# Optimization experiments

Hardware: AMD Instinct MI355X
Metric: run time of the kernel (lower is better)

## Reference

```python
import jax, jax.numpy as jnp
import numpy as np

B = 4096
DIM = 2048
B1 = 25   # root children (level-2 inner nodes)
B2 = 40   # leaves per level-2 node
NUM_CLASSES = B1 * B2  # 1000


def setup_inputs() -> dict:
    key = jax.random.key(0)
    k1, k2, k3, k4 = jax.random.split(key, 4)
    x = jax.random.normal(k1, (B, DIM), dtype=jnp.float32)
    labels = jax.random.randint(k2, (B,), 0, NUM_CLASSES, dtype=jnp.int64)
    # per-node Linear(dim, num_child + 1); column 0 = 'not in subtree'
    W_root = jax.random.normal(k3, (DIM, B1 + 1), dtype=jnp.float32) * 0.02
    b_root = jnp.zeros((B1 + 1,), dtype=jnp.float32)
    W_lvl2 = jax.random.normal(k4, (B1, DIM, B2 + 1), dtype=jnp.float32) * 0.02
    b_lvl2 = jnp.zeros((B1, B2 + 1), dtype=jnp.float32)
    return {"x": x, "labels": labels, "W_root": W_root, "b_root": b_root,
            "W_lvl2": W_lvl2, "b_lvl2": b_lvl2}


def reference(x, labels, W_root, b_root, W_lvl2, b_lvl2):
    b = x.shape[0]
    b1 = W_lvl2.shape[0]
    b2 = W_lvl2.shape[2] - 1

    # layer 1: root classifier (root.path_prob == 1.0)
    root_logits = x @ W_root + b_root                       # [B, b1+1]
    root_lp = jax.nn.log_softmax(root_logits, axis=-1)
    root_prob = jnp.exp(root_lp)

    # layer 2: all level-2 node classifiers as one grouped GEMM
    lvl2_logits = jnp.einsum('bd,ndk->bnk', x, W_lvl2) + b_lvl2  # [B, b1, b2+1]
    lvl2_lp = jax.nn.log_softmax(lvl2_logits, axis=-1)
    lvl2_prob = jnp.exp(lvl2_lp)

    # leaf path_prob = P(child under node n) * P(node n under root);
    # leaves tile out columns contiguously (label2id of complete tree)
    out = (lvl2_prob[:, :, 1:] * root_prob[:, 1:, None]).reshape(b, b1 * b2)

    # penalty: CE at each inner node divided by its layer l
    j = labels // b2                                        # level-2 parent index
    i = labels % b2                                         # leaf index within parent
    ce_root = -jnp.take_along_axis(root_lp, (j + 1)[:, None], axis=1).mean()
    # sub-label for node n: i+1 if label's parent is n, else 0
    sub_lab = jnp.where(j[:, None] == jnp.arange(b1)[None, :], (i + 1)[:, None], 0)
    gathered = jnp.take_along_axis(lvl2_lp, sub_lab[:, :, None], axis=2)[..., 0]  # [B, b1]
    penalty = ce_root + (-gathered).mean(axis=0).sum() / 2.0

    return out, penalty
```

## Files before the change

### kernel.cpp

```cpp
#include <hip/hip_runtime.h>
#include <stdint.h>

#define TB 256

typedef __bf16 bf16x8 __attribute__((ext_vector_type(8)));
typedef float f32x4 __attribute__((ext_vector_type(4)));

#define AS1 __attribute__((address_space(1)))
#define AS3 __attribute__((address_space(3)))
#define GLOAD16(gp, lp) __builtin_amdgcn_global_load_lds( \
    (const AS1 unsigned int*)(gp), (AS3 unsigned int*)(lp), 16, 0, 0)

__device__ __forceinline__ unsigned short f2bf(float f) {
  uint32_t u = __builtin_bit_cast(uint32_t, f);
  u += 0x7fffu + ((u >> 16) & 1u);
  return (unsigned short)(u >> 16);
}

__device__ __forceinline__ void waitbar3() {
  __builtin_amdgcn_sched_barrier(0);
  asm volatile("s_waitcnt vmcnt(3) lgkmcnt(0)" ::: "memory");
  __builtin_amdgcn_s_barrier();
  __builtin_amdgcn_sched_barrier(0);
}
__device__ __forceinline__ void waitbar0() {
  __builtin_amdgcn_sched_barrier(0);
  asm volatile("s_waitcnt vmcnt(0) lgkmcnt(0)" ::: "memory");
  __builtin_amdgcn_s_barrier();
  __builtin_amdgcn_sched_barrier(0);
}

__global__ __launch_bounds__(TB) void k_prep(const float* __restrict__ x,
                                             const float* __restrict__ wl,
                                             const float* __restrict__ wr,
                                             const int* __restrict__ labraw,
                                             unsigned short* __restrict__ xbf,
                                             unsigned short* __restrict__ wlt,
                                             unsigned short* __restrict__ wrt,
                                             int* __restrict__ lab32,
                                             float* __restrict__ pengl) {
  int bid = blockIdx.x, t = threadIdx.x;
  if (bid < 4096) {
    int idx = bid * TB + t;
    const float4* xin = reinterpret_cast<const float4*>(x);
    float4 a = xin[idx * 2], b = xin[idx * 2 + 1];
    uint32_t p0 = f2bf(a.x) | ((uint32_t)f2bf(a.y) << 16);
    uint32_t p1 = f2bf(a.z) | ((uint32_t)f2bf(a.w) << 16);
    uint32_t p2 = f2bf(b.x) | ((uint32_t)f2bf(b.y) << 16);
    uint32_t p3 = f2bf(b.z) | ((uint32_t)f2bf(b.w) << 16);
    reinterpret_cast<uint4*>(xbf)[idx] = make_uint4(p0, p1, p2, p3);
  } else if (bid < 4928) {
    __shared__ float ld_f[2624];
    int b2 = bid - 4096;
    if (b2 < 800) {
      int n = b2 / 32, dt = b2 % 32, d0 = dt * 64;
      const float* src = wl + ((size_t)n * 2048 + d0) * 41;
      for (int i = 0; i < 11; i++) { int lin = t + TB * i; if (lin < 2624) ld_f[lin] = src[lin]; }
      __syncthreads();
      unsigned short* dst = wlt + (size_t)n * 48 * 2048 + d0;
      for (int i = 0; i < 12; i++) {
        int lin = t + TB * i;
        int wc = lin >> 6, d = lin & 63;
        float v = (wc < 41) ? ld_f[d * 41 + wc] : 0.f;
        dst[(size_t)wc * 2048 + d] = f2bf(v);
      }
    } else {
      int dt = b2 - 800, d0 = dt * 64;
      const float* src = wr + (size_t)d0 * 26;
      for (int i = 0; i < 7; i++) { int lin = t + TB * i; if (lin < 1664) ld_f[lin] = src[lin]; }
      __syncthreads();
      unsigned short* dst = wrt + d0;
      for (int i = 0; i < 8; i++) {
        int lin = t + TB * i;
        int wc = lin >> 6, d = lin & 63;
        float v = (wc < 26) ? ld_f[d * 26 + wc] : 0.f;
        dst[(size_t)wc * 2048 + d] = f2bf(v);
      }
    }
  } else if (bid == 4928) {
    __shared__ int orred;
    if (t == 0) { orred = 0; pengl[0] = 0.f; }
    __syncthreads();
    int acc = 0;
    for (int i = t; i < 2048; i += TB) acc |= labraw[2 * i + 1];
    atomicOr(&orred, acc);
    __syncthreads();
    bool i64 = (orred == 0);
    for (int i = t; i < 4096; i += TB) lab32[i] = i64 ? labraw[2 * i] : labraw[i];
  } else {
    uint4* p = reinterpret_cast<uint4*>(wlt + (size_t)25 * 48 * 2048);
    uint4 z = make_uint4(0, 0, 0, 0);
    for (int i = t; i < 12288; i += TB) p[i] = z;
  }
}

__global__ __launch_bounds__(512) void k_root(const unsigned short* __restrict__ xbf,
                                              const unsigned short* __restrict__ wrt,
                                              const float* __restrict__ br,
                                              const int* __restrict__ labels,
                                              float* __restrict__ rootp,
                                              float* __restrict__ pengl) {
  __shared__ __align__(16) unsigned char lds3[3][24576];
  int r0 = blockIdx.x * 16;
  int tid = threadIdx.x, lane = tid & 63, wave = tid >> 6;
  int lq = lane >> 4, lr = lane & 15;
  const unsigned short* xg = xbf + (size_t)r0 * 2048;
  f32x4 acc[2] = {};

#define STAGE_RT(lb, kk)                                                              \
  do {                                                                                \
    {                                                    \
      int row = tid >> 5, s = tid & 31;                                               \
      const unsigned short* gp = xg + (size_t)row * 2048 + (kk) + ((s ^ row) << 3);   \
      GLOAD16(gp, (lb) + (size_t)tid * 16);                                           \
    }                                                                                 \
    _Pragma("unroll")                                                                 \
    for (int i = 0; i < 2; i++) {                       \
      int idx = i * 512 + tid;                                                        \
      int wc = idx >> 5, s = idx & 31;                                                \
      const unsigned short* gp = wrt + (size_t)wc * 2048 + (kk) + ((s ^ (wc & 31)) << 3); \
      GLOAD16(gp, (lb) + 8192 + (size_t)idx * 16);                                    \
    }                                                                                 \
  } while (0)

#define COMPUTE_RT(base)                                                              \
  do {                                                                                \
    int g = (wave << 2) | lq;                      \
    bf16x8 af[2], bx;                                                                 \
    _Pragma("unroll")                                                                 \
    for (int mt = 0; mt < 2; mt++) {                                                  \
      int c = mt * 16 + lr;                                                           \
      af[mt] = *reinterpret_cast<const bf16x8*>((base) + 8192 + c * 512 + ((g ^ (c & 31)) << 4)); \
    }                                                                                 \
    bx = *reinterpret_cast<const bf16x8*>((base) + lr * 512 + ((g ^ lr) << 4));       \
    _Pragma("unroll")                                                                 \
    for (int mt = 0; mt < 2; mt++)                                                    \
      acc[mt] = __builtin_amdgcn_mfma_f32_16x16x32_bf16(af[mt], bx, acc[mt], 0, 0, 0); \
  } while (0)

  STAGE_RT(&lds3[0][0], 0);
  STAGE_RT(&lds3[1][0], 256);
  waitbar3();
  int cur = 0;
#pragma unroll 3
  for (int t = 0; t < 6; ++t) {
    int nx = cur + 2; if (nx >= 3) nx -= 3;
    STAGE_RT(&lds3[nx][0], (t + 2) * 256);
    COMPUTE_RT(&lds3[cur][0]);
    waitbar3();
    ++cur; if (cur == 3) cur = 0;
  }
  COMPUTE_RT(&lds3[cur][0]);
  waitbar0();
  ++cur; if (cur == 3) cur = 0;
  COMPUTE_RT(&lds3[cur][0]);
  __syncthreads();

  float* red = (float*)&lds3[0][0];
  int li = (wave * 64 + lane) * 8;
#pragma unroll
  for (int mt = 0; mt < 2; mt++)
#pragma unroll
    for (int r = 0; r < 4; r++) red[li + mt * 4 + r] = acc[mt][r];
  __syncthreads();
  if (wave == 0) {
    float lg[2][4];
    float m = -1e30f;
#pragma unroll
    for (int mt = 0; mt < 2; mt++)
#pragma unroll
      for (int r = 0; r < 4; r++) {
        float v = 0.f;
#pragma unroll
        for (int w = 0; w < 8; w++) v += red[(w * 64 + lane) * 8 + mt * 4 + r];
        int wc = mt * 16 + lq * 4 + r;
        v += (wc < 26) ? br[wc] : -1e30f;
        lg[mt][r] = v;
        m = fmaxf(m, v);
      }
    m = fmaxf(m, __shfl_xor(m, 16));
    m = fmaxf(m, __shfl_xor(m, 32));
    float s = 0.f;
#pragma unroll
    for (int mt = 0; mt < 2; mt++)
#pragma unroll
      for (int r = 0; r < 4; r++) s += expf(lg[mt][r] - m);
    s += __shfl_xor(s, 16);
    s += __shfl_xor(s, 32);
    float ls = logf(s);
    int b = r0 + lr;
    int lab = labels[b];
    int j = lab / 40;
    float pen = 0.f;
#pragma unroll
    for (int mt = 0; mt < 2; mt++)
#pragma unroll
      for (int r = 0; r < 4; r++) {
        int wc = mt * 16 + lq * 4 + r;
        float lp = lg[mt][r] - m - ls;
        if (wc < 26) rootp[(size_t)b * 32 + wc] = expf(lp);
        if (wc == j + 1) pen -= lp;
      }
    for (int off = 32; off; off >>= 1) pen += __shfl_down(pen, off);
    if (lane == 0) atomicAdd(pengl, pen * (1.f / 4096.f));
  }
}

__global__ __launch_bounds__(TB) void k_lvl2(const unsigned short* __restrict__ xbf,
                                             const unsigned short* __restrict__ wlt,
                                             const float* __restrict__ bl,
                                             const int* __restrict__ labels,
                                             const float* __restrict__ rootp,
                                             float* __restrict__ out,
                                             float* __restrict__ pengl) {
  __shared__ __align__(16) unsigned char ldsb[2][28672];
  int bid = blockIdx.x;
  int swz = (bid & 7) * 52 + (bid >> 3);
  int rt = swz / 13, gp = swz % 13;
  int r0 = rt * 128, n0 = gp * 2;
  int tid = threadIdx.x, lane = tid & 63, wave = tid >> 6;
  int wr = wave >> 1, wcq = wave & 1;
  int lq = lane >> 4, lr = lane & 15;
  f32x4 acc[3][4] = {};
  const unsigned short* xg = xbf + (size_t)r0 * 2048;
  const unsigned short* wg = wlt + (size_t)n0 * 48 * 2048;

#define STAGE_L2(lb, kk)                                                              \
  do {                                                                                \
    _Pragma("unroll")                                                                 \
    for (int i = 0; i < 4; i++) {                                 \
      int idx = i * 256 + tid;                                                        \
      int row = idx >> 3, s = idx & 7;                                                \
      const unsigned short* gp = xg + (size_t)row * 2048 + (kk) + ((s ^ (row & 7)) << 3); \
      GLOAD16(gp, (lb) + (size_t)idx * 16);                                           \
    }                                                                                 \
    _Pragma("unroll")                                                                 \
    for (int i = 0; i < 3; i++) {                        \
      int idx = i * 256 + tid;                                                        \
      int wc = idx >> 3, s = idx & 7;                                                 \
      const unsigned short* gp = wg + (size_t)wc * 2048 + (kk) + ((s ^ (wc & 7)) << 3); \
      GLOAD16(gp, (lb) + 16384 + (size_t)idx * 16);                                   \
    }                                                                                 \
  } while (0)

#define COMPUTE_L2(base)                                                              \
  do {                                                                                \
    _Pragma("unroll")                                                                 \
    for (int ks = 0; ks < 2; ks++) {                                                  \
      int g = (ks << 2) | lq;                                                         \
      bf16x8 af[3], bx[4];                                                            \
      _Pragma("unroll")                                                               \
      for (int mt = 0; mt < 3; mt++) {                                                \
        int c = wcq * 48 + mt * 16 + lr;                                              \
        af[mt] = *reinterpret_cast<const bf16x8*>((base) + 16384 + c * 128 + ((g ^ (c & 7)) << 4)); \
      }                                                                               \
      _Pragma("unroll")                                                               \
      for (int nt = 0; nt < 4; nt++) {                                                \
        int row = wr * 64 + nt * 16 + lr;                                             \
        bx[nt] = *reinterpret_cast<const bf16x8*>((base) + row * 128 + ((g ^ (row & 7)) << 4)); \
      }                                                                               \
      _Pragma("unroll")                                                               \
      for (int mt = 0; mt < 3; mt++)                                                  \
        _Pragma("unroll")                                                             \
        for (int nt = 0; nt < 4; nt++)                                                \
          acc[mt][nt] = __builtin_amdgcn_mfma_f32_16x16x32_bf16(af[mt], bx[nt], acc[mt][nt], 0, 0, 0); \
    }                                                                                 \
  } while (0)

  STAGE_L2(&ldsb[0][0], 0);
  waitbar0();
#pragma unroll 2
  for (int t = 0; t < 32; ++t) {
    if (t < 31) STAGE_L2(&ldsb[(t + 1) & 1][0], (t + 1) * 64);
    COMPUTE_L2(&ldsb[t & 1][0]);
    waitbar0();
  }

  int n = n0 + wcq;
  bool valid = (n < 25);
  float bb[3][4];
#pragma unroll
  for (int mt = 0; mt < 3; mt++)
#pragma unroll
    for (int r = 0; r < 4; r++) {
      int wcg = mt * 16 + lq * 4 + r;
      bb[mt][r] = (valid && wcg < 41) ? bl[n * 41 + wcg] : -1e30f;
    }
  float pen = 0.f;
#pragma unroll
  for (int nt = 0; nt < 4; nt++) {
    int b = r0 + wr * 64 + nt * 16 + lr;
    float lg[3][4];
    float m = -1e30f;
#pragma unroll
    for (int mt = 0; mt < 3; mt++)
#pragma unroll
      for (int r = 0; r < 4; r++) {
        float v = acc[mt][nt][r] + bb[mt][r];
        lg[mt][r] = v;
        m = fmaxf(m, v);
      }
    m = fmaxf(m, __shfl_xor(m, 16));
    m = fmaxf(m, __shfl_xor(m, 32));
    float s = 0.f;
#pragma unroll
    for (int mt = 0; mt < 3; mt++)
#pragma unroll
      for (int r = 0; r < 4; r++) s += expf(lg[mt][r] - m);
    s += __shfl_xor(s, 16);
    s += __shfl_xor(s, 32);
    float ls = logf(s);
    float rp = valid ? rootp[(size_t)b * 32 + (n + 1)] : 0.f;
    int lab = labels[b];
    int j = lab / 40;
    int sub = (j == n) ? (lab - j * 40 + 1) : 0;
#pragma unroll
    for (int mt = 0; mt < 3; mt++)
#pragma unroll
      for (int r = 0; r < 4; r++) {
        int wcg = mt * 16 + lq * 4 + r;
        float lp = lg[mt][r] - m - ls;
        if (valid && wcg >= 1 && wcg < 41) out[(size_t)b * 1000 + n * 40 + wcg - 1] = expf(lp) * rp;
        if (valid && wcg == sub) pen -= lp;
      }
  }
  for (int off = 32; off; off >>= 1) pen += __shfl_down(pen, off);
  float* red = (float*)&ldsb[0][0];
  if (lane == 0) red[wave] = pen;
  __syncthreads();
  if (tid == 0) atomicAdd(pengl, (red[0] + red[1] + red[2] + red[3]) * (1.f / 8192.f));
}

extern "C" void kernel_launch(void* const* d_in, const int* in_sizes, int n_in,
                              void* d_out, int out_size, void* d_ws, size_t ws_size,
                              hipStream_t stream) {
  const float* x = (const float*)d_in[0];
  const int* labels_raw = (const int*)d_in[1];
  const float* wroot = (const float*)d_in[2];
  const float* broot = (const float*)d_in[3];
  const float* wlvl2 = (const float*)d_in[4];
  const float* blvl2 = (const float*)d_in[5];
  float* out = (float*)d_out;
  float* pengl = out + 4096000;

  char* ws = (char*)d_ws;
  unsigned short* xbf = (unsigned short*)ws;
  unsigned short* wlt = (unsigned short*)(ws + 16777216);
  unsigned short* wrt = (unsigned short*)(ws + 21889024);
  float* rootp = (float*)(ws + 22020096);
  int* lab32 = (int*)(ws + 22544384);

  k_prep<<<4930, TB, 0, stream>>>(x, wlvl2, wroot, labels_raw, xbf, wlt, wrt, lab32, pengl);
  k_root<<<256, 512, 0, stream>>>(xbf, wrt, broot, lab32, rootp, pengl);
  k_lvl2<<<416, TB, 0, stream>>>(xbf, wlt, blvl2, lab32, rootp, out, pengl);
}
```

Measured before the change: 147.3 us.

## Widen lvl2 GEMM tile to four nodes and triple-buffer LDS pipeline

The level-2 grouped GEMM block now covers four node classifiers (192 weight columns) per 128-row tile with 512 threads, instead of two nodes with 256 threads. The grid shrinks from 416 to 224 blocks, and the weights are padded to 28 groups. The K loop moves from double buffering with a full vmcnt(0) wait to a three-stage LDS ring that waits with vmcnt(5), so two loads stay in flight during compute. The aim is to reuse each x tile across more weight columns and to hide global-load latency. The cost is about 120KB of LDS per block, which limits occupancy to one block per CU, and fewer blocks than the 256 CUs.

```diff
diff --git a/kernel.cpp b/kernel.cpp
--- a/kernel.cpp
+++ b/kernel.cpp
@@ -17,6 +17,12 @@
   return (unsigned short)(u >> 16);
 }
 
+__device__ __forceinline__ void waitbar5() {
+  __builtin_amdgcn_sched_barrier(0);
+  asm volatile("s_waitcnt vmcnt(5) lgkmcnt(0)" ::: "memory");
+  __builtin_amdgcn_s_barrier();
+  __builtin_amdgcn_sched_barrier(0);
+}
 __device__ __forceinline__ void waitbar3() {
   __builtin_amdgcn_sched_barrier(0);
   asm volatile("s_waitcnt vmcnt(3) lgkmcnt(0)" ::: "memory");
@@ -88,7 +94,8 @@
     bool i64 = (orred == 0);
     for (int i = t; i < 4096; i += TB) lab32[i] = i64 ? labraw[2 * i] : labraw[i];
   } else {
-    uint4* p = reinterpret_cast<uint4*>(wlt + (size_t)25 * 48 * 2048);
+    int g = 25 + (bid - 4929);
+    uint4* p = reinterpret_cast<uint4*>(wlt + (size_t)g * 48 * 2048);
     uint4 z = make_uint4(0, 0, 0, 0);
     for (int i = t; i < 12288; i += TB) p[i] = z;
   }
@@ -206,20 +213,20 @@
   }
 }
 
-__global__ __launch_bounds__(TB) void k_lvl2(const unsigned short* __restrict__ xbf,
-                                             const unsigned short* __restrict__ wlt,
-                                             const float* __restrict__ bl,
-                                             const int* __restrict__ labels,
-                                             const float* __restrict__ rootp,
-                                             float* __restrict__ out,
-                                             float* __restrict__ pengl) {
-  __shared__ __align__(16) unsigned char ldsb[2][28672];
+__global__ __launch_bounds__(512) void k_lvl2(const unsigned short* __restrict__ xbf,
+                                              const unsigned short* __restrict__ wlt,
+                                              const float* __restrict__ bl,
+                                              const int* __restrict__ labels,
+                                              const float* __restrict__ rootp,
+                                              float* __restrict__ out,
+                                              float* __restrict__ pengl) {
+  __shared__ __align__(16) unsigned char lds3[3][40960];
   int bid = blockIdx.x;
-  int swz = (bid & 7) * 52 + (bid >> 3);
-  int rt = swz / 13, gp = swz % 13;
-  int r0 = rt * 128, n0 = gp * 2;
+  int swz = (bid & 7) * 28 + (bid >> 3);
+  int rt = swz / 7, quad = swz % 7;
+  int r0 = rt * 128, n0 = quad * 4;
   int tid = threadIdx.x, lane = tid & 63, wave = tid >> 6;
-  int wr = wave >> 1, wcq = wave & 1;
+  int wr = wave >> 2, wcq = wave & 3;
   int lq = lane >> 4, lr = lane & 15;
   f32x4 acc[3][4] = {};
   const unsigned short* xg = xbf + (size_t)r0 * 2048;
@@ -228,15 +235,15 @@
 #define STAGE_L2(lb, kk)                                                              \
   do {                                                                                \
     _Pragma("unroll")                                                                 \
-    for (int i = 0; i < 4; i++) {                                 \
-      int idx = i * 256 + tid;                                                        \
+    for (int i = 0; i < 2; i++) {                                 \
+      int idx = i * 512 + tid;                                                        \
       int row = idx >> 3, s = idx & 7;                                                \
       const unsigned short* gp = xg + (size_t)row * 2048 + (kk) + ((s ^ (row & 7)) << 3); \
       GLOAD16(gp, (lb) + (size_t)idx * 16);                                           \
     }                                                                                 \
     _Pragma("unroll")                                                                 \
-    for (int i = 0; i < 3; i++) {                        \
-      int idx = i * 256 + tid;                                                        \
+    for (int i = 0; i < 3; i++) {                      \
+      int idx = i * 512 + tid;                                                        \
       int wc = idx >> 3, s = idx & 7;                                                 \
       const unsigned short* gp = wg + (size_t)wc * 2048 + (kk) + ((s ^ (wc & 7)) << 3); \
       GLOAD16(gp, (lb) + 16384 + (size_t)idx * 16);                                   \
@@ -267,14 +274,22 @@
     }                                                                                 \
   } while (0)
 
-  STAGE_L2(&ldsb[0][0], 0);
+  STAGE_L2(&lds3[0][0], 0);
+  STAGE_L2(&lds3[1][0], 64);
+  waitbar5();
+  int cur = 0;
+#pragma unroll 3
+  for (int t = 0; t < 30; ++t) {
+    int nx = cur + 2; if (nx >= 3) nx -= 3;
+    STAGE_L2(&lds3[nx][0], (t + 2) * 64);
+    COMPUTE_L2(&lds3[cur][0]);
+    waitbar5();
+    ++cur; if (cur == 3) cur = 0;
+  }
+  COMPUTE_L2(&lds3[cur][0]);
   waitbar0();
-#pragma unroll 2
-  for (int t = 0; t < 32; ++t) {
-    if (t < 31) STAGE_L2(&ldsb[(t + 1) & 1][0], (t + 1) * 64);
-    COMPUTE_L2(&ldsb[t & 1][0]);
-    waitbar0();
-  }
+  ++cur; if (cur == 3) cur = 0;
+  COMPUTE_L2(&lds3[cur][0]);
 
   int n = n0 + wcq;
   bool valid = (n < 25);
@@ -325,10 +340,15 @@
       }
   }
   for (int off = 32; off; off >>= 1) pen += __shfl_down(pen, off);
-  float* red = (float*)&ldsb[0][0];
+  float* red = (float*)&lds3[0][0];
   if (lane == 0) red[wave] = pen;
   __syncthreads();
-  if (tid == 0) atomicAdd(pengl, (red[0] + red[1] + red[2] + red[3]) * (1.f / 8192.f));
+  if (tid == 0) {
+    float tot = 0.f;
+#pragma unroll
+    for (int w = 0; w < 8; w++) tot += red[w];
+    atomicAdd(pengl, tot * (1.f / 8192.f));
+  }
 }
 
 extern "C" void kernel_launch(void* const* d_in, const int* in_sizes, int n_in,
@@ -346,11 +366,11 @@
   char* ws = (char*)d_ws;
   unsigned short* xbf = (unsigned short*)ws;
   unsigned short* wlt = (unsigned short*)(ws + 16777216);
-  unsigned short* wrt = (unsigned short*)(ws + 21889024);
-  float* rootp = (float*)(ws + 22020096);
-  int* lab32 = (int*)(ws + 22544384);
-
-  k_prep<<<4930, TB, 0, stream>>>(x, wlvl2, wroot, labels_raw, xbf, wlt, wrt, lab32, pengl);
+  unsigned short* wrt = (unsigned short*)(ws + 22282240);
+  float* rootp = (float*)(ws + 22413312);
+  int* lab32 = (int*)(ws + 22937600);
+
+  k_prep<<<4932, TB, 0, stream>>>(x, wlvl2, wroot, labels_raw, xbf, wlt, wrt, lab32, pengl);
   k_root<<<256, 512, 0, stream>>>(xbf, wrt, broot, lab32, rootp, pengl);
-  k_lvl2<<<416, TB, 0, stream>>>(xbf, wlt, blvl2, lab32, rootp, out, pengl);
-}
+  k_lvl2<<<224, 512, 0, stream>>>(xbf, wlt, blvl2, lab32, rootp, out, pengl);
+}
```

Result: no change. 149.7 us (+1.6%).

## Widen level-2 GEMM tile to four node groups per block

Applied to the files above, without the earlier changes.

Each k_lvl2 block now covers four level-2 node classifiers (192 weight columns) instead of two. This halves the number of blocks and the redundant re-loading of the x tile across node groups. It grows the accumulators to 6x4 MFMA tiles, raises LDS use per block to about 80KB, and pads the weight buffer with three zeroed groups. The grid drops to 224 blocks, under one wave across the CUs, and the custom waitcnt barrier is replaced by __syncthreads, which may reduce occupancy and load overlap.

```diff
diff --git a/kernel.cpp b/kernel.cpp
--- a/kernel.cpp
+++ b/kernel.cpp
@@ -88,7 +88,8 @@
     bool i64 = (orred == 0);
     for (int i = t; i < 4096; i += TB) lab32[i] = i64 ? labraw[2 * i] : labraw[i];
   } else {
-    uint4* p = reinterpret_cast<uint4*>(wlt + (size_t)25 * 48 * 2048);
+    int g = 25 + (bid - 4929);
+    uint4* p = reinterpret_cast<uint4*>(wlt + (size_t)g * 48 * 2048);
     uint4 z = make_uint4(0, 0, 0, 0);
     for (int i = t; i < 12288; i += TB) p[i] = z;
   }
@@ -206,39 +207,39 @@
   }
 }
 
-__global__ __launch_bounds__(TB) void k_lvl2(const unsigned short* __restrict__ xbf,
-                                             const unsigned short* __restrict__ wlt,
-                                             const float* __restrict__ bl,
-                                             const int* __restrict__ labels,
-                                             const float* __restrict__ rootp,
-                                             float* __restrict__ out,
-                                             float* __restrict__ pengl) {
-  __shared__ __align__(16) unsigned char ldsb[2][28672];
+__global__ __launch_bounds__(TB, 2) void k_lvl2(const unsigned short* __restrict__ xbf,
+                                                const unsigned short* __restrict__ wlt,
+                                                const float* __restrict__ bl,
+                                                const int* __restrict__ labels,
+                                                const float* __restrict__ rootp,
+                                                float* __restrict__ out,
+                                                float* __restrict__ pengl) {
+  __shared__ __align__(16) unsigned char ldsb[2][40960];
   int bid = blockIdx.x;
-  int swz = (bid & 7) * 52 + (bid >> 3);
-  int rt = swz / 13, gp = swz % 13;
-  int r0 = rt * 128, n0 = gp * 2;
+  int swz = (bid & 7) * 28 + (bid >> 3);
+  int rt = swz / 7, quad = swz % 7;
+  int r0 = rt * 128, n0 = quad * 4;
   int tid = threadIdx.x, lane = tid & 63, wave = tid >> 6;
-  int wr = wave >> 1, wcq = wave & 1;
+  int wr = wave >> 1, wc = wave & 1;
   int lq = lane >> 4, lr = lane & 15;
-  f32x4 acc[3][4] = {};
+  f32x4 acc[6][4] = {};
   const unsigned short* xg = xbf + (size_t)r0 * 2048;
   const unsigned short* wg = wlt + (size_t)n0 * 48 * 2048;
 
 #define STAGE_L2(lb, kk)                                                              \
   do {                                                                                \
     _Pragma("unroll")                                                                 \
-    for (int i = 0; i < 4; i++) {                                 \
+    for (int i = 0; i < 4; i++) {                      \
       int idx = i * 256 + tid;                                                        \
       int row = idx >> 3, s = idx & 7;                                                \
       const unsigned short* gp = xg + (size_t)row * 2048 + (kk) + ((s ^ (row & 7)) << 3); \
       GLOAD16(gp, (lb) + (size_t)idx * 16);                                           \
     }                                                                                 \
     _Pragma("unroll")                                                                 \
-    for (int i = 0; i < 3; i++) {                        \
+    for (int i = 0; i < 6; i++) {                      \
       int idx = i * 256 + tid;                                                        \
-      int wc = idx >> 3, s = idx & 7;                                                 \
-      const unsigned short* gp = wg + (size_t)wc * 2048 + (kk) + ((s ^ (wc & 7)) << 3); \
+      int wrow = idx >> 3, s = idx & 7;                                               \
+      const unsigned short* gp = wg + (size_t)wrow * 2048 + (kk) + ((s ^ (wrow & 7)) << 3); \
       GLOAD16(gp, (lb) + 16384 + (size_t)idx * 16);                                   \
     }                                                                                 \
   } while (0)
@@ -248,10 +249,10 @@
     _Pragma("unroll")                                                                 \
     for (int ks = 0; ks < 2; ks++) {                                                  \
       int g = (ks << 2) | lq;                                                         \
-      bf16x8 af[3], bx[4];                                                            \
+      bf16x8 af[6], bx[4];                                                            \
       _Pragma("unroll")                                                               \
-      for (int mt = 0; mt < 3; mt++) {                                                \
-        int c = wcq * 48 + mt * 16 + lr;                                              \
+      for (int mt = 0; mt < 6; mt++) {                                                \
+        int c = wc * 96 + mt * 16 + lr;                                               \
         af[mt] = *reinterpret_cast<const bf16x8*>((base) + 16384 + c * 128 + ((g ^ (c & 7)) << 4)); \
       }                                                                               \
       _Pragma("unroll")                                                               \
@@ -260,7 +261,7 @@
         bx[nt] = *reinterpret_cast<const bf16x8*>((base) + row * 128 + ((g ^ (row & 7)) << 4)); \
       }                                                                               \
       _Pragma("unroll")                                                               \
-      for (int mt = 0; mt < 3; mt++)                                                  \
+      for (int mt = 0; mt < 6; mt++)                                                  \
         _Pragma("unroll")                                                             \
         for (int nt = 0; nt < 4; nt++)                                                \
           acc[mt][nt] = __builtin_amdgcn_mfma_f32_16x16x32_bf16(af[mt], bx[nt], acc[mt][nt], 0, 0, 0); \
@@ -268,61 +269,64 @@
   } while (0)
 
   STAGE_L2(&ldsb[0][0], 0);
-  waitbar0();
+  __syncthreads();
 #pragma unroll 2
   for (int t = 0; t < 32; ++t) {
     if (t < 31) STAGE_L2(&ldsb[(t + 1) & 1][0], (t + 1) * 64);
     COMPUTE_L2(&ldsb[t & 1][0]);
-    waitbar0();
-  }
-
-  int n = n0 + wcq;
-  bool valid = (n < 25);
-  float bb[3][4];
-#pragma unroll
-  for (int mt = 0; mt < 3; mt++)
-#pragma unroll
-    for (int r = 0; r < 4; r++) {
-      int wcg = mt * 16 + lq * 4 + r;
-      bb[mt][r] = (valid && wcg < 41) ? bl[n * 41 + wcg] : -1e30f;
+    __syncthreads();
+  }
+
+  float pen = 0.f;
+#pragma unroll
+  for (int gi = 0; gi < 2; gi++) {
+    int n = n0 + 2 * wc + gi;
+    bool valid = (n < 25);
+    float bb[3][4];
+#pragma unroll
+    for (int q = 0; q < 3; q++)
+#pragma unroll
+      for (int r = 0; r < 4; r++) {
+        int wcg = q * 16 + lq * 4 + r;
+        bb[q][r] = (valid && wcg < 41) ? bl[n * 41 + wcg] : -1e30f;
+      }
+#pragma unroll
+    for (int nt = 0; nt < 4; nt++) {
+      int b = r0 + wr * 64 + nt * 16 + lr;
+      float lg[3][4];
+      float m = -1e30f;
+#pragma unroll
+      for (int q = 0; q < 3; q++)
+#pragma unroll
+        for (int r = 0; r < 4; r++) {
+          float v = acc[gi * 3 + q][nt][r] + bb[q][r];
+          lg[q][r] = v;
+          m = fmaxf(m, v);
+        }
+      m = fmaxf(m, __shfl_xor(m, 16));
+      m = fmaxf(m, __shfl_xor(m, 32));
+      float s = 0.f;
+#pragma unroll
+      for (int q = 0; q < 3; q++)
+#pragma unroll
+        for (int r = 0; r < 4; r++) s += expf(lg[q][r] - m);
+      s += __shfl_xor(s, 16);
+      s += __shfl_xor(s, 32);
+      float ls = logf(s);
+      float rp = valid ? rootp[(size_t)b * 32 + (n + 1)] : 0.f;
+      int lab = labels[b];
+      int j = lab / 40;
+      int sub = (j == n) ? (lab - j * 40 + 1) : 0;
+#pragma unroll
+      for (int q = 0; q < 3; q++)
+#pragma unroll
+        for (int r = 0; r < 4; r++) {
+          int wcg = q * 16 + lq * 4 + r;
+          float lp = lg[q][r] - m - ls;
+          if (valid && wcg >= 1 && wcg < 41) out[(size_t)b * 1000 + n * 40 + wcg - 1] = expf(lp) * rp;
+          if (valid && wcg == sub) pen -= lp;
+        }
     }
-  float pen = 0.f;
-#pragma unroll
-  for (int nt = 0; nt < 4; nt++) {
-    int b = r0 + wr * 64 + nt * 16 + lr;
-    float lg[3][4];
-    float m = -1e30f;
-#pragma unroll
-    for (int mt = 0; mt < 3; mt++)
-#pragma unroll
-      for (int r = 0; r < 4; r++) {
-        float v = acc[mt][nt][r] + bb[mt][r];
-        lg[mt][r] = v;
-        m = fmaxf(m, v);
-      }
-    m = fmaxf(m, __shfl_xor(m, 16));
-    m = fmaxf(m, __shfl_xor(m, 32));
-    float s = 0.f;
-#pragma unroll
-    for (int mt = 0; mt < 3; mt++)
-#pragma unroll
-      for (int r = 0; r < 4; r++) s += expf(lg[mt][r] - m);
-    s += __shfl_xor(s, 16);
-    s += __shfl_xor(s, 32);
-    float ls = logf(s);
-    float rp = valid ? rootp[(size_t)b * 32 + (n + 1)] : 0.f;
-    int lab = labels[b];
-    int j = lab / 40;
-    int sub = (j == n) ? (lab - j * 40 + 1) : 0;
-#pragma unroll
-    for (int mt = 0; mt < 3; mt++)
-#pragma unroll
-      for (int r = 0; r < 4; r++) {
-        int wcg = mt * 16 + lq * 4 + r;
-        float lp = lg[mt][r] - m - ls;
-        if (valid && wcg >= 1 && wcg < 41) out[(size_t)b * 1000 + n * 40 + wcg - 1] = expf(lp) * rp;
-        if (valid && wcg == sub) pen -= lp;
-      }
   }
   for (int off = 32; off; off >>= 1) pen += __shfl_down(pen, off);
   float* red = (float*)&ldsb[0][0];
@@ -346,11 +350,11 @@
   char* ws = (char*)d_ws;
   unsigned short* xbf = (unsigned short*)ws;
   unsigned short* wlt = (unsigned short*)(ws + 16777216);
-  unsigned short* wrt = (unsigned short*)(ws + 21889024);
-  float* rootp = (float*)(ws + 22020096);
-  int* lab32 = (int*)(ws + 22544384);
-
-  k_prep<<<4930, TB, 0, stream>>>(x, wlvl2, wroot, labels_raw, xbf, wlt, wrt, lab32, pengl);
+  unsigned short* wrt = (unsigned short*)(ws + 22282240);
+  float* rootp = (float*)(ws + 22413312);
+  int* lab32 = (int*)(ws + 22937600);
+
+  k_prep<<<4932, TB, 0, stream>>>(x, wlvl2, wroot, labels_raw, xbf, wlt, wrt, lab32, pengl);
   k_root<<<256, 512, 0, stream>>>(xbf, wrt, broot, lab32, rootp, pengl);
-  k_lvl2<<<416, TB, 0, stream>>>(xbf, wlt, blvl2, lab32, rootp, out, pengl);
-}
+  k_lvl2<<<224, TB, 0, stream>>>(xbf, wlt, blvl2, lab32, rootp, out, pengl);
+}
```

Measured after the change: 159.1 us. +8.0%, slower.
